# Performance work log

Measured on AMD Instinct MI355X. Metric: run time of the kernel, lower is better.

Reference implementation:

```python
import jax, jax.numpy as jnp
import numpy as np

N_HEADS = 8

def setup_inputs() -> dict:
    key = jax.random.key(0)
    k0, k1, k2, k3, k4 = jax.random.split(key, 5)
    B, S, D = 2, 2048, 1024
    scale = 0.02
    return {
        "x": jax.random.normal(k0, (B, S, D), dtype=jnp.float32),
        "Wk": jax.random.normal(k1, (D, D), dtype=jnp.float32) * scale,
        "Wv": jax.random.normal(k2, (D, D), dtype=jnp.float32) * scale,
        "Wself": jax.random.normal(k3, (D, D), dtype=jnp.float32) * scale,
        "Wout": jax.random.normal(k4, (D, D), dtype=jnp.float32) * scale,
    }

def reference(x, Wk, Wv, Wself, Wout):
    B, S, D = x.shape
    H = N_HEADS
    hd = D // H
    # torch Linear: y = x @ W.T (no bias)
    keys = (x @ Wk.T).reshape(B, S, H, hd).transpose(0, 2, 1, 3)  # [B,H,S,hd]
    vals = (x @ Wv.T).reshape(B, S, H, hd).transpose(0, 2, 1, 3)  # [B,H,S,hd]
    # energy = K K^T / sqrt(hd); weights = softmax(-energy) with causal mask
    neg_energy = -jnp.einsum("bhqd,bhkd->bhqk", keys, keys) / jnp.sqrt(
        jnp.asarray(hd, dtype=x.dtype))
    causal = jnp.tril(jnp.ones((S, S), dtype=bool))  # allowed positions
    neg_energy = jnp.where(causal, neg_energy, -jnp.inf)
    weights = jax.nn.softmax(neg_energy, axis=-1)  # [B,H,S,S]
    pairwise = jnp.einsum("bhqk,bhkd->bhqd", weights, vals)
    pairwise = pairwise.transpose(0, 2, 1, 3).reshape(B, S, D)
    self_force = x @ Wself.T
    return (pairwise + self_force) @ Wout.T
```

## Files before the change

### kernel.cpp

```cpp
#include <hip/hip_runtime.h>


typedef unsigned short u16;
typedef short s16x8 __attribute__((ext_vector_type(8)));
typedef short s16x4 __attribute__((ext_vector_type(4)));
typedef unsigned short u16x4 __attribute__((ext_vector_type(4)));
typedef unsigned short u16x8 __attribute__((ext_vector_type(8)));
typedef float f32x4 __attribute__((ext_vector_type(4)));

#define DEV __device__ __forceinline__

DEV u16 f2bf(float f) {
    union { float f; unsigned u; } v; v.f = f;
    return (u16)((v.u + 0x7FFFu + ((v.u >> 16) & 1u)) >> 16);
}
DEV float bf2f(u16 h) {
    union { unsigned u; float f; } v; v.u = ((unsigned)h) << 16;
    return v.f;
}
DEV void gload16(const void* g, void* l) {
    __builtin_amdgcn_global_load_lds(
        (const __attribute__((address_space(1))) void*)g,
        (__attribute__((address_space(3))) void*)l, 16, 0, 0);
}

#define FULL_BARRIER()                          \
    do {                                        \
        __builtin_amdgcn_sched_barrier(0);      \
        __builtin_amdgcn_s_barrier();           \
        __builtin_amdgcn_sched_barrier(0);      \
    } while (0)

__global__ __launch_bounds__(256) void cast_all(
    const float* __restrict__ x, const float* __restrict__ wk,
    const float* __restrict__ wv, const float* __restrict__ wsf,
    const float* __restrict__ wo,
    u16* __restrict__ xb, u16* __restrict__ wkb, u16* __restrict__ wvb,
    u16* __restrict__ wsb, u16* __restrict__ wob) {
    int i = blockIdx.x * 256 + threadIdx.x;
    const int NX = (2 * 2048 * 1024) / 4;
    const int NW = (1024 * 1024) / 4;
    const float* src; u16* dst; int off;
    if (i < NX)              { src = x;   dst = xb;  off = i; }
    else if (i < NX + NW)    { src = wk;  dst = wkb; off = i - NX; }
    else if (i < NX + 2*NW)  { src = wv;  dst = wvb; off = i - NX - NW; }
    else if (i < NX + 3*NW)  { src = wsf; dst = wsb; off = i - NX - 2*NW; }
    else                     { src = wo;  dst = wob; off = i - NX - 3*NW; }
    float4 v = ((const float4*)src)[off];
    u16x4 o = { f2bf(v.x), f2bf(v.y), f2bf(v.z), f2bf(v.w) };
    ((u16x4*)dst)[off] = o;
}

template <int MODE>
__global__ __launch_bounds__(256, 2) void gemm_big(
    const u16* __restrict__ A, const u16* __restrict__ W,
    u16* __restrict__ Kb, u16* __restrict__ Vtb, u16* __restrict__ Sbf,
    float* __restrict__ Of) {
    constexpr int BM = (MODE == 0) ? 256 : 128;
    constexpr int MF = BM / 64;
    __shared__ __align__(16) u16 As[2][BM * 32];
    __shared__ __align__(16) u16 Bs[2][128 * 32];
    const int tid = threadIdx.x, lane = tid & 63, wave = tid >> 6;
    const int hi = lane >> 4, lo = lane & 15;
    const int m0 = blockIdx.y * BM, n0 = blockIdx.x * 128;

    f32x4 acc[MF][8];
#pragma unroll
    for (int i = 0; i < MF; ++i)
#pragma unroll
        for (int j = 0; j < 8; ++j) acc[i][j] = f32x4{0.f, 0.f, 0.f, 0.f};

    const u16* asrc[MF]; int adst[MF];
#pragma unroll
    for (int q = 0; q < MF; ++q) {
        int p = wave * (MF * 1024) + q * 1024 + lane * 16;
        adst[q] = wave * (MF * 1024) + q * 1024;
        int rw = p >> 6, cb = (p & 63) ^ (((rw >> 1) & 3) << 4);
        asrc[q] = A + ((size_t)(m0 + rw) << 10) + (cb >> 1);
    }
    const u16* bsrc[2]; int bdst[2];
#pragma unroll
    for (int q = 0; q < 2; ++q) {
        int p = wave * 2048 + q * 1024 + lane * 16;
        bdst[q] = wave * 2048 + q * 1024;
        int rw = p >> 6, cb = (p & 63) ^ (((rw >> 1) & 3) << 4);
        bsrc[q] = W + ((size_t)(n0 + rw) << 10) + (cb >> 1);
    }
    auto stage = [&](int k0, int buf) {
#pragma unroll
        for (int q = 0; q < MF; ++q) gload16(asrc[q] + k0, (char*)As[buf] + adst[q]);
#pragma unroll
        for (int q = 0; q < 2; ++q) gload16(bsrc[q] + k0, (char*)Bs[buf] + bdst[q]);
    };

    stage(0, 0);
    const int hb = hi << 4;
    for (int t = 0; t < 32; ++t) {
        const int cur = t & 1;
        asm volatile("s_waitcnt vmcnt(0)" ::: "memory");
        FULL_BARRIER();
        if (t < 31) stage((t + 1) << 5, cur ^ 1);
        s16x8 af[MF], bfr[8];
#pragma unroll
        for (int i = 0; i < MF; ++i) {
            int rw = wave * (MF * 16) + i * 16 + lo;
            af[i] = *(const s16x8*)((const char*)As[cur] + rw * 64 + (hb ^ (((rw >> 1) & 3) << 4)));
        }
#pragma unroll
        for (int j = 0; j < 8; ++j) {
            int rw = j * 16 + lo;
            bfr[j] = *(const s16x8*)((const char*)Bs[cur] + rw * 64 + (hb ^ (((rw >> 1) & 3) << 4)));
        }
#pragma unroll
        for (int i = 0; i < MF; ++i)
#pragma unroll
            for (int j = 0; j < 8; ++j)
                acc[i][j] = __builtin_amdgcn_mfma_f32_16x16x32_bf16(af[i], bfr[j], acc[i][j], 0, 0, 0);
    }

    if (MODE == 1) {
#pragma unroll
        for (int i = 0; i < MF; ++i)
#pragma unroll
            for (int j = 0; j < 8; ++j) {
                int n = n0 + j * 16 + lo;
                int mbase = m0 + wave * (MF * 16) + i * 16 + (hi << 2);
#pragma unroll
                for (int r = 0; r < 4; ++r)
                    Of[((size_t)(mbase + r) << 10) + n] = acc[i][j][r];
            }
    } else {
        const int seg = n0 >> 10, nn0 = n0 & 1023;
        if (seg == 1) {
#pragma unroll
            for (int i = 0; i < MF; ++i)
#pragma unroll
                for (int j = 0; j < 8; ++j) {
                    int n = nn0 + j * 16 + lo;
                    int h = n >> 7, d = n & 127;
                    int mbase = m0 + wave * (MF * 16) + i * 16 + (hi << 2);
                    int b = mbase >> 11, s = mbase & 2047;
                    u16x4 pk;
#pragma unroll
                    for (int r = 0; r < 4; ++r) pk[r] = f2bf(acc[i][j][r]);
                    *(u16x4*)(Vtb + (((size_t)(b * 8 + h) << 7) + d) * 2048 + s) = pk;
                }
        } else {
            u16* dst = seg ? Sbf : Kb;
#pragma unroll
            for (int i = 0; i < MF; ++i)
#pragma unroll
                for (int j = 0; j < 8; ++j) {
                    int n = nn0 + j * 16 + lo;
                    int mbase = m0 + wave * (MF * 16) + i * 16 + (hi << 2);
#pragma unroll
                    for (int r = 0; r < 4; ++r)
                        dst[((size_t)(mbase + r) << 10) + n] = f2bf(acc[i][j][r]);
                }
        }
    }
}

#define MINIT (-30000.0f)
#define MASKV (-60000.0f)
__global__ __launch_bounds__(256, 4) void attn_split(
    const u16* __restrict__ Kb, const u16* __restrict__ Vtb,
    u16* __restrict__ Op0, u16* __restrict__ Op1,
    float* __restrict__ Mp, float* __restrict__ Lp) {
    __shared__ __align__(16) u16 Ks[2][32 * 128];
    __shared__ __align__(16) u16 Vs[2][128 * 32];
    const int tid = threadIdx.x, lane = tid & 63, wave = tid >> 6;
    const int q_raw = blockIdx.x >> 1, half = blockIdx.x & 1;
    const int bh = blockIdx.y, b = bh >> 3, h = bh & 7;
    const int qt = ((bh >> 2) & 1) ? q_raw : (31 - q_raw);
    const int hi = lane >> 4, lo = lane & 15;
    const int qrow = qt * 64 + wave * 16 + lo;

    s16x8 qf[4];
    {
        const u16* qp = Kb + ((size_t)(b * 2048 + qrow) << 10) + h * 128 + (hi << 3);
#pragma unroll
        for (int c = 0; c < 4; ++c) qf[c] = *(const s16x8*)(qp + c * 32);
    }

    const u16* ksrc[2];
    const u16* vsrc[2];
    int ldst[2];
#pragma unroll
    for (int jj = 0; jj < 2; ++jj) {
        int p = wave * 2048 + jj * 1024 + lane * 16;
        ldst[jj] = wave * 2048 + jj * 1024;
        int rk = p >> 8, cbs = (p & 255) ^ ((rk & 7) << 4);
        ksrc[jj] = Kb + ((size_t)(b * 2048 + rk) << 10) + h * 128 + (cbs >> 1);
        int dv = p >> 6, kbs = (p & 63) ^ ((dv & 3) << 4);
        vsrc[jj] = Vtb + (((size_t)(bh * 128 + dv)) << 11) + (kbs >> 1);
    }
    auto stage = [&](int ks0, int buf) {
        char* kb = (char*)Ks[buf];
        char* vb = (char*)Vs[buf];
#pragma unroll
        for (int jj = 0; jj < 2; ++jj) {
            gload16(ksrc[jj] + ((size_t)ks0 << 10), kb + ldst[jj]);
            gload16(vsrc[jj] + ks0, vb + ldst[jj]);
        }
    };

    f32x4 oacc[8];
#pragma unroll
    for (int nf = 0; nf < 8; ++nf) oacc[nf] = f32x4{0.f, 0.f, 0.f, 0.f};
    float mrun = MINIT, lrun = 0.f;
    const float SC = -0.12751741566723328f;

    const int j0 = half ? (qt + 1) : 0;
    const int j1 = j0 + qt + 1;

    stage(j0 << 5, 0);
    for (int j = j0; j < j1; ++j) {
        const int cur = (j - j0) & 1;
        asm volatile("s_waitcnt vmcnt(0)" ::: "memory");
        FULL_BARRIER();
        if (j + 1 < j1) stage((j + 1) << 5, cur ^ 1);

        f32x4 sf[2];
        __builtin_amdgcn_s_setprio(1);
#pragma unroll
        for (int mf = 0; mf < 2; ++mf) {
            f32x4 s = {0.f, 0.f, 0.f, 0.f};
            int kr = mf * 16 + lo;
            const char* rowp = (const char*)Ks[cur] + kr * 256;
            int swz = (kr & 7) << 4;
#pragma unroll
            for (int c = 0; c < 4; ++c) {
                s16x8 kf = *(const s16x8*)(rowp + ((c * 64 + hi * 16) ^ swz));
                s = __builtin_amdgcn_mfma_f32_16x16x32_bf16(kf, qf[c], s, 0, 0, 0);
            }
            sf[mf] = s;
        }
        __builtin_amdgcn_s_setprio(0);

        const bool diag = (j >= 2 * qt);
        float p[2][4];
        float pm = MASKV;
#pragma unroll
        for (int mf = 0; mf < 2; ++mf)
#pragma unroll
            for (int r = 0; r < 4; ++r) {
                float sv = sf[mf][r] * SC;
                if (diag) {
                    int kg = j * 32 + mf * 16 + (hi << 2) + r;
                    if (kg > qrow) sv = MASKV;
                }
                p[mf][r] = sv;
                pm = fmaxf(pm, sv);
            }
        pm = fmaxf(pm, __shfl_xor(pm, 16));
        pm = fmaxf(pm, __shfl_xor(pm, 32));

        const bool grow = !__all(pm <= mrun);
        float mnew = mrun;
        if (grow) {
            mnew = fmaxf(mrun, pm);
            float corr = exp2f(mrun - mnew);
            lrun *= corr;
            float cr[4];
#pragma unroll
            for (int r = 0; r < 4; ++r) cr[r] = __shfl(corr, (hi << 2) + r);
#pragma unroll
            for (int nf = 0; nf < 8; ++nf)
#pragma unroll
                for (int r = 0; r < 4; ++r) oacc[nf][r] *= cr[r];
            mrun = mnew;
        }

        float psum = 0.f;
        float p2[2][4];
#pragma unroll
        for (int mf = 0; mf < 2; ++mf)
#pragma unroll
            for (int r = 0; r < 4; ++r) {
                float e = exp2f(p[mf][r] - mnew);
                p2[mf][r] = e;
                psum += e;
            }
        psum += __shfl_xor(psum, 16);
        psum += __shfl_xor(psum, 32);
        lrun += psum;

        unsigned pw0, pw1, pw2, pw3;
        asm("v_cvt_pk_bf16_f32 %0, %1, %2" : "=v"(pw0) : "v"(p2[0][0]), "v"(p2[0][1]));
        asm("v_cvt_pk_bf16_f32 %0, %1, %2" : "=v"(pw1) : "v"(p2[0][2]), "v"(p2[0][3]));
        asm("v_cvt_pk_bf16_f32 %0, %1, %2" : "=v"(pw2) : "v"(p2[1][0]), "v"(p2[1][1]));
        asm("v_cvt_pk_bf16_f32 %0, %1, %2" : "=v"(pw3) : "v"(p2[1][2]), "v"(p2[1][3]));
        union { unsigned w[4]; s16x8 v; } pau;
        pau.w[0] = pw0; pau.w[1] = pw1; pau.w[2] = pw2; pau.w[3] = pw3;
        s16x8 pa = pau.v;

        __builtin_amdgcn_s_setprio(1);
#pragma unroll
        for (int nf = 0; nf < 8; ++nf) {
            int d = nf * 16 + lo;
            const char* vrow = (const char*)Vs[cur] + d * 64;
            int swz = (d & 3) << 4;
            int ob = hi << 3;
            s16x4 vlo = *(const s16x4*)(vrow + (ob ^ swz));
            s16x4 vhi = *(const s16x4*)(vrow + ((ob + 32) ^ swz));
            s16x8 vf = {vlo[0], vlo[1], vlo[2], vlo[3], vhi[0], vhi[1], vhi[2], vhi[3]};
            oacc[nf] = __builtin_amdgcn_mfma_f32_16x16x32_bf16(pa, vf, oacc[nf], 0, 0, 0);
        }
        __builtin_amdgcn_s_setprio(0);
    }

    if (hi == 0) {
        int mi = (half * 16 + bh) * 2048 + qrow;
        Mp[mi] = mrun;
        Lp[mi] = lrun;
    }
    u16* Op = half ? Op1 : Op0;
#pragma unroll
    for (int nf = 0; nf < 8; ++nf) {
        int d = nf * 16 + lo;
#pragma unroll
        for (int r = 0; r < 4; ++r) {
            int q2 = qt * 64 + wave * 16 + (hi << 2) + r;
            Op[((size_t)(b * 2048 + q2) << 10) + h * 128 + d] = f2bf(oacc[nf][r]);
        }
    }
}

__global__ __launch_bounds__(256) void attn_combine(
    const u16* __restrict__ O0, const u16* __restrict__ O1,
    const float* __restrict__ Mp, const float* __restrict__ Lp,
    const u16* __restrict__ Sb, u16* __restrict__ Tb) {
    int i = blockIdx.x * 256 + threadIdx.x;
    int d0 = (i & 15) << 3;
    int row = i >> 4;
    int h = row & 7;
    int bq = row >> 3;
    int b = bq >> 11, q = bq & 2047;
    int bh = b * 8 + h;
    int mi0 = bh * 2048 + q, mi1 = (16 + bh) * 2048 + q;
    float m0 = Mp[mi0], m1 = Mp[mi1], l0 = Lp[mi0], l1 = Lp[mi1];
    float m = fmaxf(m0, m1);
    float a0 = exp2f(m0 - m), a1 = exp2f(m1 - m);
    float rd = 1.0f / (l0 * a0 + l1 * a1);
    size_t base = ((size_t)bq << 10) + (h << 7) + d0;
    s16x8 o0 = *(const s16x8*)(O0 + base);
    s16x8 o1 = *(const s16x8*)(O1 + base);
    s16x8 sf = *(const s16x8*)(Sb + base);
    u16x8 out;
#pragma unroll
    for (int e = 0; e < 8; ++e)
        out[e] = f2bf((bf2f((u16)o0[e]) * a0 + bf2f((u16)o1[e]) * a1) * rd + bf2f((u16)sf[e]));
    *(u16x8*)(Tb + base) = out;
}

extern "C" void kernel_launch(void* const* d_in, const int* in_sizes, int n_in,
                              void* d_out, int out_size, void* d_ws, size_t ws_size,
                              hipStream_t stream) {
    const float* x   = (const float*)d_in[0];
    const float* Wk  = (const float*)d_in[1];
    const float* Wv  = (const float*)d_in[2];
    const float* Wsf = (const float*)d_in[3];
    const float* Wo  = (const float*)d_in[4];
    float* out = (float*)d_out;
    char* ws = (char*)d_ws;
    u16* xb   = (u16*)(ws);
    u16* wcat = (u16*)(ws + (8u << 20));
    u16* Kb   = (u16*)(ws + (16u << 20));
    u16* Vtb  = (u16*)(ws + (24u << 20));
    u16* Sbf  = (u16*)(ws + (32u << 20));
    u16* Tb   = xb;

    u16* wob   = (u16*)(ws + (40u << 20));
    u16* Op0   = xb;
    u16* Op1   = (u16*)(ws + (8u << 20));
    float* Mp  = (float*)(ws + (42u << 20));
    float* Lp  = (float*)(ws + (42u << 20) + (256u << 10));

    cast_all<<<8192, 256, 0, stream>>>(x, Wk, Wv, Wsf, Wo,
                                       xb, wcat, wcat + (1u << 20), wcat + (2u << 20), wob);
    gemm_big<0><<<dim3(24, 16), 256, 0, stream>>>(xb, wcat, Kb, Vtb, Sbf, nullptr);
    attn_split<<<dim3(64, 16), 256, 0, stream>>>(Kb, Vtb, Op0, Op1, Mp, Lp);
    attn_combine<<<2048, 256, 0, stream>>>(Op0, Op1, Mp, Lp, Sbf, Tb);
    gemm_big<1><<<dim3(8, 32), 256, 0, stream>>>(Tb, wob, nullptr, nullptr, nullptr, out);
}
```

Baseline: 227.5 us.

## Rewrite QKV projection GEMM as 8-wave 256x256 tile with interleaved loads

Replaces the fused K/V/self projection GEMM with a 512-thread, 8-wave kernel that uses 256x256 output tiles and BK=64 with XOR-swizzled LDS. It interleaves global-to-LDS staging of the next tile with MFMA phases and uses setprio and partial vmcnt waits so loads overlap compute. It also remaps workgroup ids in an XCD-aware order. The output GEMM is split into its own non-templated kernel with unchanged logic. The cost is heavy LDS use (128KB per block) and complex barrier choreography that can limit occupancy or stall if the phases are mistimed.

```diff
diff --git a/kernel.cpp b/kernel.cpp
--- a/kernel.cpp
+++ b/kernel.cpp
@@ -29,6 +29,12 @@
         __builtin_amdgcn_sched_barrier(0);      \
         __builtin_amdgcn_s_barrier();           \
         __builtin_amdgcn_sched_barrier(0);      \
+    } while (0)
+
+#define LGKM0_FENCE()                                        \
+    do {                                                     \
+        asm volatile("s_waitcnt lgkmcnt(0)" ::: "memory");   \
+        __builtin_amdgcn_sched_barrier(0);                   \
     } while (0)
 
 __global__ __launch_bounds__(256) void cast_all(
@@ -51,30 +57,180 @@
     ((u16x4*)dst)[off] = o;
 }
 
-template <int MODE>
-__global__ __launch_bounds__(256, 2) void gemm_big(
+__global__ __launch_bounds__(512, 2) void gemm8_proj(
     const u16* __restrict__ A, const u16* __restrict__ W,
-    u16* __restrict__ Kb, u16* __restrict__ Vtb, u16* __restrict__ Sbf,
+    u16* __restrict__ Kb, u16* __restrict__ Vtb, u16* __restrict__ Sbf) {
+    __shared__ __align__(16) u16 As[2][256 * 64];
+    __shared__ __align__(16) u16 Bs[2][256 * 64];
+    const int tid = threadIdx.x, lane = tid & 63, wave = tid >> 6;
+    const int hi = lane >> 4, lo = lane & 15;
+    const int wr = wave >> 2, wc = wave & 3;
+
+    const int nwg = gridDim.x, cpx = nwg >> 3, o = blockIdx.x;
+    const int wg = (o & 7) * cpx + (o >> 3);
+    const int bm = wg & 15, bn = wg >> 4;
+    const int m0 = bm << 8, n0 = bn << 8;
+
+    f32x4 acc[8][4];
+#pragma unroll
+    for (int i = 0; i < 8; ++i)
+#pragma unroll
+        for (int j = 0; j < 4; ++j) acc[i][j] = f32x4{0.f, 0.f, 0.f, 0.f};
+
+    const u16* sp[8];
+    int ldst[8];
+#pragma unroll
+    for (int hh = 0; hh < 4; ++hh)
+#pragma unroll
+        for (int q = 0; q < 2; ++q) {
+            int seg = wave * 2 + q;
+            int p = seg * 1024 + lane * 16;
+            int lr = p >> 7, c = (p >> 4) & 7;
+            int r = ((hh & 1) << 7) + lr;
+            int cl = c ^ (r & 7);
+            const u16* base = (hh < 2) ? (A + ((size_t)(m0 + r) << 10))
+                                       : (W + ((size_t)(n0 + r) << 10));
+            sp[hh * 2 + q] = base + (cl << 3);
+            ldst[hh * 2 + q] = ((hh & 1) << 14) + seg * 1024;
+        }
+
+    auto stageH = [&](int hh, int k0, int buf) {
+        char* dst = (hh < 2) ? (char*)As[buf] : (char*)Bs[buf];
+#pragma unroll
+        for (int q = 0; q < 2; ++q)
+            gload16(sp[hh * 2 + q] + k0, dst + ldst[hh * 2 + q]);
+    };
+    auto readA = [&](int buf, int i, int kk) -> s16x8 {
+        int r = (wr << 7) + (i << 4) + lo;
+        int cl = (kk << 2) + hi;
+        return *(const s16x8*)((const char*)As[buf] + r * 128 + ((cl ^ (r & 7)) << 4));
+    };
+    auto readB = [&](int buf, int j, int kk) -> s16x8 {
+        int r = (wc << 6) + (j << 4) + lo;
+        int cl = (kk << 2) + hi;
+        return *(const s16x8*)((const char*)Bs[buf] + r * 128 + ((cl ^ (r & 7)) << 4));
+    };
+
+    auto ktile = [&](int buf, int k0, int sk0, bool ds, bool last) {
+        s16x8 alo[4], ahi[4], b0[4], b1[4];
+#pragma unroll
+        for (int i = 0; i < 4; ++i) { alo[i] = readA(buf, i, 0); ahi[i] = readA(buf, i, 1); }
+#pragma unroll
+        for (int j = 0; j < 4; ++j) b0[j] = readB(buf, j, 0);
+        FULL_BARRIER();
+        LGKM0_FENCE();
+        __builtin_amdgcn_s_setprio(1);
+#pragma unroll
+        for (int i = 0; i < 4; ++i)
+#pragma unroll
+            for (int j = 0; j < 4; ++j)
+                acc[i][j] = __builtin_amdgcn_mfma_f32_16x16x32_bf16(alo[i], b0[j], acc[i][j], 0, 0, 0);
+        __builtin_amdgcn_s_setprio(0);
+        FULL_BARRIER();
+#pragma unroll
+        for (int j = 0; j < 4; ++j) b1[j] = readB(buf, j, 1);
+        FULL_BARRIER();
+        LGKM0_FENCE();
+        __builtin_amdgcn_s_setprio(1);
+#pragma unroll
+        for (int i = 0; i < 4; ++i)
+#pragma unroll
+            for (int j = 0; j < 4; ++j)
+                acc[i][j] = __builtin_amdgcn_mfma_f32_16x16x32_bf16(ahi[i], b1[j], acc[i][j], 0, 0, 0);
+        __builtin_amdgcn_s_setprio(0);
+        FULL_BARRIER();
+#pragma unroll
+        for (int i = 0; i < 4; ++i) { alo[i] = readA(buf, i + 4, 0); ahi[i] = readA(buf, i + 4, 1); }
+        if (ds) stageH(2, sk0, buf);
+        FULL_BARRIER();
+        LGKM0_FENCE();
+        __builtin_amdgcn_s_setprio(1);
+#pragma unroll
+        for (int i = 0; i < 4; ++i)
+#pragma unroll
+            for (int j = 0; j < 4; ++j)
+                acc[i + 4][j] = __builtin_amdgcn_mfma_f32_16x16x32_bf16(alo[i], b0[j], acc[i + 4][j], 0, 0, 0);
+        __builtin_amdgcn_s_setprio(0);
+        FULL_BARRIER();
+        if (ds) { stageH(3, sk0, buf); stageH(0, sk0, buf); stageH(1, sk0, buf); }
+        FULL_BARRIER();
+        LGKM0_FENCE();
+        __builtin_amdgcn_s_setprio(1);
+#pragma unroll
+        for (int i = 0; i < 4; ++i)
+#pragma unroll
+            for (int j = 0; j < 4; ++j)
+                acc[i + 4][j] = __builtin_amdgcn_mfma_f32_16x16x32_bf16(ahi[i], b1[j], acc[i + 4][j], 0, 0, 0);
+        __builtin_amdgcn_s_setprio(0);
+        if (!last) asm volatile("s_waitcnt vmcnt(8)" ::: "memory");
+        else       asm volatile("s_waitcnt vmcnt(0)" ::: "memory");
+        FULL_BARRIER();
+    };
+
+#pragma unroll
+    for (int hh = 0; hh < 4; ++hh) stageH(hh, 0, 0);
+#pragma unroll
+    for (int hh = 0; hh < 4; ++hh) stageH(hh, 64, 1);
+    asm volatile("s_waitcnt vmcnt(8)" ::: "memory");
+    FULL_BARRIER();
+
+    for (int it = 0; it < 8; ++it) {
+        const bool ds = it < 7, last = it == 7;
+        ktile(0, (2 * it) * 64,     (2 * it + 2) * 64, ds, last);
+        ktile(1, (2 * it + 1) * 64, (2 * it + 3) * 64, ds, last);
+    }
+
+    const int seg = n0 >> 10, nn0 = (n0 & 1023) + wc * 64;
+    const int mb = m0 + wr * 128;
+    if (seg == 1) {
+#pragma unroll
+        for (int i = 0; i < 8; ++i)
+#pragma unroll
+            for (int j = 0; j < 4; ++j) {
+                int n = nn0 + j * 16 + lo;
+                int h = n >> 7, d = n & 127;
+                int mbase = mb + i * 16 + (hi << 2);
+                int b = mbase >> 11, s = mbase & 2047;
+                u16x4 pk;
+#pragma unroll
+                for (int r = 0; r < 4; ++r) pk[r] = f2bf(acc[i][j][r]);
+                *(u16x4*)(Vtb + (((size_t)(b * 8 + h) << 7) + d) * 2048 + s) = pk;
+            }
+    } else {
+        u16* dst = seg ? Sbf : Kb;
+#pragma unroll
+        for (int i = 0; i < 8; ++i)
+#pragma unroll
+            for (int j = 0; j < 4; ++j) {
+                int n = nn0 + j * 16 + lo;
+                int mbase = mb + i * 16 + (hi << 2);
+#pragma unroll
+                for (int r = 0; r < 4; ++r)
+                    dst[((size_t)(mbase + r) << 10) + n] = f2bf(acc[i][j][r]);
+            }
+    }
+}
+
+__global__ __launch_bounds__(256, 2) void gemm_out(
+    const u16* __restrict__ A, const u16* __restrict__ W,
     float* __restrict__ Of) {
-    constexpr int BM = (MODE == 0) ? 256 : 128;
-    constexpr int MF = BM / 64;
-    __shared__ __align__(16) u16 As[2][BM * 32];
+    __shared__ __align__(16) u16 As[2][128 * 32];
     __shared__ __align__(16) u16 Bs[2][128 * 32];
     const int tid = threadIdx.x, lane = tid & 63, wave = tid >> 6;
     const int hi = lane >> 4, lo = lane & 15;
-    const int m0 = blockIdx.y * BM, n0 = blockIdx.x * 128;
-
-    f32x4 acc[MF][8];
-#pragma unroll
-    for (int i = 0; i < MF; ++i)
+    const int m0 = blockIdx.y * 128, n0 = blockIdx.x * 128;
+
+    f32x4 acc[2][8];
+#pragma unroll
+    for (int i = 0; i < 2; ++i)
 #pragma unroll
         for (int j = 0; j < 8; ++j) acc[i][j] = f32x4{0.f, 0.f, 0.f, 0.f};
 
-    const u16* asrc[MF]; int adst[MF];
-#pragma unroll
-    for (int q = 0; q < MF; ++q) {
-        int p = wave * (MF * 1024) + q * 1024 + lane * 16;
-        adst[q] = wave * (MF * 1024) + q * 1024;
+    const u16* asrc[2]; int adst[2];
+#pragma unroll
+    for (int q = 0; q < 2; ++q) {
+        int p = wave * 2048 + q * 1024 + lane * 16;
+        adst[q] = wave * 2048 + q * 1024;
         int rw = p >> 6, cb = (p & 63) ^ (((rw >> 1) & 3) << 4);
         asrc[q] = A + ((size_t)(m0 + rw) << 10) + (cb >> 1);
     }
@@ -88,7 +244,7 @@
     }
     auto stage = [&](int k0, int buf) {
 #pragma unroll
-        for (int q = 0; q < MF; ++q) gload16(asrc[q] + k0, (char*)As[buf] + adst[q]);
+        for (int q = 0; q < 2; ++q) gload16(asrc[q] + k0, (char*)As[buf] + adst[q]);
 #pragma unroll
         for (int q = 0; q < 2; ++q) gload16(bsrc[q] + k0, (char*)Bs[buf] + bdst[q]);
     };
@@ -100,10 +256,10 @@
         asm volatile("s_waitcnt vmcnt(0)" ::: "memory");
         FULL_BARRIER();
         if (t < 31) stage((t + 1) << 5, cur ^ 1);
-        s16x8 af[MF], bfr[8];
-#pragma unroll
-        for (int i = 0; i < MF; ++i) {
-            int rw = wave * (MF * 16) + i * 16 + lo;
+        s16x8 af[2], bfr[8];
+#pragma unroll
+        for (int i = 0; i < 2; ++i) {
+            int rw = wave * 32 + i * 16 + lo;
             af[i] = *(const s16x8*)((const char*)As[cur] + rw * 64 + (hb ^ (((rw >> 1) & 3) << 4)));
         }
 #pragma unroll
@@ -112,53 +268,21 @@
             bfr[j] = *(const s16x8*)((const char*)Bs[cur] + rw * 64 + (hb ^ (((rw >> 1) & 3) << 4)));
         }
 #pragma unroll
-        for (int i = 0; i < MF; ++i)
+        for (int i = 0; i < 2; ++i)
 #pragma unroll
             for (int j = 0; j < 8; ++j)
                 acc[i][j] = __builtin_amdgcn_mfma_f32_16x16x32_bf16(af[i], bfr[j], acc[i][j], 0, 0, 0);
     }
-
-    if (MODE == 1) {
-#pragma unroll
-        for (int i = 0; i < MF; ++i)
-#pragma unroll
-            for (int j = 0; j < 8; ++j) {
-                int n = n0 + j * 16 + lo;
-                int mbase = m0 + wave * (MF * 16) + i * 16 + (hi << 2);
-#pragma unroll
-                for (int r = 0; r < 4; ++r)
-                    Of[((size_t)(mbase + r) << 10) + n] = acc[i][j][r];
-            }
-    } else {
-        const int seg = n0 >> 10, nn0 = n0 & 1023;
-        if (seg == 1) {
-#pragma unroll
-            for (int i = 0; i < MF; ++i)
-#pragma unroll
-                for (int j = 0; j < 8; ++j) {
-                    int n = nn0 + j * 16 + lo;
-                    int h = n >> 7, d = n & 127;
-                    int mbase = m0 + wave * (MF * 16) + i * 16 + (hi << 2);
-                    int b = mbase >> 11, s = mbase & 2047;
-                    u16x4 pk;
-#pragma unroll
-                    for (int r = 0; r < 4; ++r) pk[r] = f2bf(acc[i][j][r]);
-                    *(u16x4*)(Vtb + (((size_t)(b * 8 + h) << 7) + d) * 2048 + s) = pk;
-                }
-        } else {
-            u16* dst = seg ? Sbf : Kb;
-#pragma unroll
-            for (int i = 0; i < MF; ++i)
-#pragma unroll
-                for (int j = 0; j < 8; ++j) {
-                    int n = nn0 + j * 16 + lo;
-                    int mbase = m0 + wave * (MF * 16) + i * 16 + (hi << 2);
-#pragma unroll
-                    for (int r = 0; r < 4; ++r)
-                        dst[((size_t)(mbase + r) << 10) + n] = f2bf(acc[i][j][r]);
-                }
-        }
-    }
+#pragma unroll
+    for (int i = 0; i < 2; ++i)
+#pragma unroll
+        for (int j = 0; j < 8; ++j) {
+            int n = n0 + j * 16 + lo;
+            int mbase = m0 + wave * 32 + i * 16 + (hi << 2);
+#pragma unroll
+            for (int r = 0; r < 4; ++r)
+                Of[((size_t)(mbase + r) << 10) + n] = acc[i][j][r];
+        }
 }
 
 #define MINIT (-30000.0f)
@@ -182,7 +306,6 @@
 #pragma unroll
         for (int c = 0; c < 4; ++c) qf[c] = *(const s16x8*)(qp + c * 32);
     }
-
     const u16* ksrc[2];
     const u16* vsrc[2];
     int ldst[2];
@@ -379,8 +502,8 @@
 
     cast_all<<<8192, 256, 0, stream>>>(x, Wk, Wv, Wsf, Wo,
                                        xb, wcat, wcat + (1u << 20), wcat + (2u << 20), wob);
-    gemm_big<0><<<dim3(24, 16), 256, 0, stream>>>(xb, wcat, Kb, Vtb, Sbf, nullptr);
+    gemm8_proj<<<192, 512, 0, stream>>>(xb, wcat, Kb, Vtb, Sbf);
     attn_split<<<dim3(64, 16), 256, 0, stream>>>(Kb, Vtb, Op0, Op1, Mp, Lp);
     attn_combine<<<2048, 256, 0, stream>>>(Op0, Op1, Mp, Lp, Sbf, Tb);
-    gemm_big<1><<<dim3(8, 32), 256, 0, stream>>>(Tb, wob, nullptr, nullptr, nullptr, out);
-}
+    gemm_out<<<dim3(8, 32), 256, 0, stream>>>(Tb, wob, out);
+}
```

After: 223.1 us. No clear change (-1.9%).
